# Optimization experiments

Measured on AMD Instinct MI355X. Metric: run time of the kernel, lower is better.

## Reference

```python
import jax, jax.numpy as jnp
import numpy as np

ATT_DIM = 128
C = 256
B, H, W = 4, 64, 64


def setup_inputs() -> dict:
    key = jax.random.key(0)
    ks = jax.random.split(key, 6)
    s = 1.0 / np.sqrt(C)
    return {
        "x": jax.random.normal(ks[0], (B, C, H, W), dtype=jnp.float32),
        "Wg": jax.random.normal(ks[1], (ATT_DIM, C), dtype=jnp.float32) * s,
        "Wf": jax.random.normal(ks[2], (ATT_DIM, C), dtype=jnp.float32) * s,
        "Wh": jax.random.normal(ks[3], (ATT_DIM, C), dtype=jnp.float32) * s,
        "Wv": jax.random.normal(ks[4], (C, ATT_DIM), dtype=jnp.float32) * (1.0 / np.sqrt(ATT_DIM)),
        "lambda_att": jax.random.normal(ks[5], (), dtype=jnp.float32),
    }


def reference(x, Wg, Wf, Wh, Wv, lambda_att):
    # x: [B, C, H, W]; 1x1 channels_first convs == channel matmuls
    b, c, h, w = x.shape
    hw = h * w
    d = Wg.shape[0]
    # project and flatten spatial dims -> tokens: [B, HW, d]
    g = jnp.einsum('dc,bchw->bhwd', Wg, x).reshape(b, hw, d)  # query
    f = jnp.einsum('dc,bchw->bhwd', Wf, x).reshape(b, hw, d)  # value
    hh = jnp.einsum('dc,bchw->bhwd', Wh, x).reshape(b, hw, d)  # key
    # keras layers.Attention([g, f, h]): scores = query @ key^T (unscaled),
    # out = softmax(scores) @ value
    scores = jnp.einsum('bqd,bkd->bqk', g, hh)  # [B, HW, HW]
    attw = jax.nn.softmax(scores, axis=-1)
    v = jnp.einsum('bqk,bkd->bqd', attw, f)  # [B, HW, d]
    # back to [B, d, H, W], project to C channels
    v = v.transpose(0, 2, 1).reshape(b, d, h, w)
    v = jnp.einsum('cd,bdhw->bchw', Wv, v)
    return x + lambda_att * v
```

## Files before the change

### kernel.cpp

```cpp
#include <hip/hip_runtime.h>

typedef _Float16 h16;
typedef __attribute__((ext_vector_type(8))) _Float16 half8;
typedef __attribute__((ext_vector_type(4))) _Float16 half4;
typedef __attribute__((ext_vector_type(4))) float f32x4;
typedef unsigned int u32;
typedef unsigned short u16;
typedef unsigned long long u64;

#define LOG2E 1.44269504088896340736f

__device__ __forceinline__ void gl_lds16(const void* g, void* l){
  __builtin_amdgcn_global_load_lds((const __attribute__((address_space(1))) u32*)g,
                                   (__attribute__((address_space(3))) u32*)l, 16, 0, 0);
}
__device__ __forceinline__ f32x4 mfma16(half8 a, half8 b, f32x4 c){
  return __builtin_amdgcn_mfma_f32_16x16x32_f16(a, b, c, 0, 0, 0);
}
__device__ __forceinline__ f32x4 fzero(){
  f32x4 z = {0.f, 0.f, 0.f, 0.f};
  return z;
}

__global__ void k_cvtw(const float* __restrict__ Wg, const float* __restrict__ Wf,
                       const float* __restrict__ Wh, const float* __restrict__ Wv,
                       h16* __restrict__ o){
  int i = blockIdx.x * 256 + threadIdx.x;
  o[i]          = (h16)Wg[i];
  o[32768 + i]  = (h16)Wf[i];
  o[65536 + i]  = (h16)Wh[i];
  o[98304 + i]  = (h16)Wv[i];
}

__global__ __launch_bounds__(256, 2)
void k_proj(const float* __restrict__ x, const h16* __restrict__ Wgb,
            const h16* __restrict__ Whb, const h16* __restrict__ Wfb,
            h16* __restrict__ Q, h16* __restrict__ K, h16* __restrict__ Vt){
  __shared__ __align__(16) char Xl[32 * 512];
  int bid = blockIdx.x;
  int b = bid >> 7, p0 = (bid & 127) * 32;
  int tid = threadIdx.x;
  int w = tid >> 6, lane = tid & 63, g4 = lane >> 4, ln = lane & 15;

  #pragma unroll
  for (int pass = 0; pass < 2; ++pass){
    int idx = pass * 256 + tid;
    int c4 = idx >> 3, p4 = idx & 7;
    const float* xp = x + ((size_t)b * 256 + c4 * 4) * 4096 + p0 + p4 * 4;
    float4 v0 = *(const float4*)(xp);
    float4 v1 = *(const float4*)(xp + 4096);
    float4 v2 = *(const float4*)(xp + 8192);
    float4 v3 = *(const float4*)(xp + 12288);
    #pragma unroll
    for (int i = 0; i < 4; ++i){
      int row = p4 * 4 + i;
      half4 v = { (h16)((&v0.x)[i]), (h16)((&v1.x)[i]),
                  (h16)((&v2.x)[i]), (h16)((&v3.x)[i]) };
      *(half4*)&Xl[row * 512 + ((c4 * 8) ^ ((row & 7) << 4))] = v;
    }
  }
  __syncthreads();

  half8 xf[2][8];
  #pragma unroll
  for (int pt = 0; pt < 2; ++pt){
    int p = pt * 16 + ln;
    #pragma unroll
    for (int ks = 0; ks < 8; ++ks)
      xf[pt][ks] = *(const half8*)&Xl[p * 512 + (((ks * 4 + g4) ^ (p & 7)) << 4)];
  }

  const h16* Ws0[3] = {Wgb, Whb, Wfb};
  #pragma unroll
  for (int mat = 0; mat < 3; ++mat){
    const h16* Wm = Ws0[mat];
    #pragma unroll
    for (int dtl = 0; dtl < 2; ++dtl){
      int drow = w * 32 + dtl * 16 + ln;
      half8 wf[8];
      #pragma unroll
      for (int ks = 0; ks < 8; ++ks)
        wf[ks] = *(const half8*)&Wm[(size_t)drow * 256 + ks * 32 + g4 * 8];
      #pragma unroll
      for (int pt = 0; pt < 2; ++pt){
        f32x4 acc = fzero();
        #pragma unroll
        for (int ks = 0; ks < 8; ++ks)
          acc = mfma16(wf[ks], xf[pt][ks], acc);
        int p = p0 + pt * 16 + ln;
        int dbase = w * 32 + dtl * 16 + g4 * 4;
        if (mat < 2){
          h16* Dst = (mat == 0) ? Q : K;
          half4 v = { (h16)acc[0], (h16)acc[1], (h16)acc[2], (h16)acc[3] };
          *(half4*)&Dst[((size_t)b * 4096 + p) * 128 + dbase] = v;
        } else {
          #pragma unroll
          for (int r = 0; r < 4; ++r)
            Vt[((size_t)b * 128 + dbase + r) * 4096 + p] = (h16)acc[r];
        }
      }
    }
  }
}

__global__ __launch_bounds__(256, 2)
void k_attn(const h16* __restrict__ Q, const h16* __restrict__ K,
            const h16* __restrict__ Vt, h16* __restrict__ Opart,
            float* __restrict__ Mb, float* __restrict__ Lb){
  __shared__ __align__(16) char Kl[2][16384];
  __shared__ __align__(16) char Vl[2][16384];
  __shared__ __align__(16) char Pl[4][4096];

  int bid = blockIdx.x;
  int b = bid >> 7, qb = (bid >> 2) & 31, sp = bid & 3;
  int tid = threadIdx.x;
  int w = tid >> 6, lane = tid & 63, g4 = lane >> 4, ln = lane & 15;
  int q0 = qb * 128 + w * 32;

  half8 qf[2][4];
  #pragma unroll
  for (int qt = 0; qt < 2; ++qt)
    #pragma unroll
    for (int ks = 0; ks < 4; ++ks)
      qf[qt][ks] = *(const half8*)&Q[((size_t)b * 4096 + q0 + qt * 16 + ln) * 128 + ks * 32 + g4 * 8];

  f32x4 acc[2][8];
  #pragma unroll
  for (int qt = 0; qt < 2; ++qt)
    #pragma unroll
    for (int dt = 0; dt < 8; ++dt)
      acc[qt][dt] = fzero();
  float mrow[2] = {-1e30f, -1e30f};
  float lrow[2] = {0.f, 0.f};

  int base0 = sp * 1024;

  auto stage = [&](int buf, int kv0){
    #pragma unroll
    for (int i = 0; i < 4; ++i){
      int off = i * 4096 + w * 1024 + lane * 16;
      int row = off >> 8, c16 = (off >> 4) & 15;
      gl_lds16(&K[((size_t)b * 4096 + kv0 + row) * 128 + ((c16 ^ (row & 7)) << 3)],
               &Kl[buf][i * 4096 + w * 1024]);
    }
    #pragma unroll
    for (int i = 0; i < 4; ++i){
      int off = i * 4096 + w * 1024 + lane * 16;
      int row = off >> 7, c16 = (off >> 4) & 7;
      gl_lds16(&Vt[((size_t)b * 128 + row) * 4096 + kv0 + ((c16 ^ (row & 7)) << 3)],
               &Vl[buf][i * 4096 + w * 1024]);
    }
  };

  stage(0, base0);
  __syncthreads();

  int cur = 0;
  for (int t = 0; t < 16; ++t){
    if (t < 15) stage(cur ^ 1, base0 + (t + 1) * 64);

    f32x4 s[4][2];
    #pragma unroll
    for (int kt = 0; kt < 4; ++kt)
      #pragma unroll
      for (int qt = 0; qt < 2; ++qt) s[kt][qt] = fzero();
    #pragma unroll
    for (int kt = 0; kt < 4; ++kt){
      int key = kt * 16 + ln;
      #pragma unroll
      for (int ks = 0; ks < 4; ++ks){
        half8 kf = *(const half8*)&Kl[cur][key * 256 + (((ks * 4 + g4) ^ (key & 7)) << 4)];
        #pragma unroll
        for (int qt = 0; qt < 2; ++qt)
          s[kt][qt] = mfma16(kf, qf[qt][ks], s[kt][qt]);
      }
    }

    #pragma unroll
    for (int qt = 0; qt < 2; ++qt){
      float mx = -1e30f;
      #pragma unroll
      for (int kt = 0; kt < 4; ++kt)
        #pragma unroll
        for (int r = 0; r < 4; ++r) mx = fmaxf(mx, s[kt][qt][r]);
      mx = fmaxf(mx, __shfl_xor(mx, 16));
      mx = fmaxf(mx, __shfl_xor(mx, 32));
      float mnew = fmaxf(mrow[qt], mx);
      float scale = exp2f((mrow[qt] - mnew) * LOG2E);
      mrow[qt] = mnew;
      float ps = 0.f;
      int q = qt * 16 + ln;
      #pragma unroll
      for (int kt = 0; kt < 4; ++kt){
        float e0 = exp2f((s[kt][qt][0] - mnew) * LOG2E);
        float e1 = exp2f((s[kt][qt][1] - mnew) * LOG2E);
        float e2 = exp2f((s[kt][qt][2] - mnew) * LOG2E);
        float e3 = exp2f((s[kt][qt][3] - mnew) * LOG2E);
        ps += (e0 + e1) + (e2 + e3);
        half4 pv = { (h16)e0, (h16)e1, (h16)e2, (h16)e3 };
        *(half4*)&Pl[w][q * 128 + ((kt * 32 + g4 * 8) ^ ((q & 7) << 4))] = pv;
      }
      ps += __shfl_xor(ps, 16);
      ps += __shfl_xor(ps, 32);
      lrow[qt] = lrow[qt] * scale + ps;
      #pragma unroll
      for (int r = 0; r < 4; ++r){
        float sc = __shfl(scale, g4 * 4 + r);
        #pragma unroll
        for (int dt = 0; dt < 8; ++dt) acc[qt][dt][r] *= sc;
      }
    }

    #pragma unroll
    for (int st = 0; st < 2; ++st){
      half8 pa[2];
      #pragma unroll
      for (int qt = 0; qt < 2; ++qt){
        int q = qt * 16 + ln;
        pa[qt] = *(const half8*)&Pl[w][q * 128 + (((st * 4 + g4) ^ (q & 7)) << 4)];
      }
      #pragma unroll
      for (int dt = 0; dt < 8; ++dt){
        int row = dt * 16 + ln;
        half8 vf = *(const half8*)&Vl[cur][row * 128 + (((st * 4 + g4) ^ (row & 7)) << 4)];
        #pragma unroll
        for (int qt = 0; qt < 2; ++qt)
          acc[qt][dt] = mfma16(pa[qt], vf, acc[qt][dt]);
      }
    }

    __syncthreads();
    cur ^= 1;
  }

  int pb = (b * 64 + qb * 2 + (w >> 1)) * 4 + sp;
  #pragma unroll
  for (int qt = 0; qt < 2; ++qt)
    #pragma unroll
    for (int dt = 0; dt < 8; ++dt)
      #pragma unroll
      for (int r = 0; r < 4; ++r){
        int qloc = (w & 1) * 32 + qt * 16 + g4 * 4 + r;
        Opart[(size_t)pb * 8192 + qloc * 128 + dt * 16 + ln] = (h16)acc[qt][dt][r];
      }
  if (lane < 16){
    #pragma unroll
    for (int qt = 0; qt < 2; ++qt){
      int qloc = (w & 1) * 32 + qt * 16 + lane;
      Mb[pb * 64 + qloc] = mrow[qt];
      Lb[pb * 64 + qloc] = lrow[qt];
    }
  }
}

__global__ __launch_bounds__(256, 4)
void k_comb(const h16* __restrict__ Opart, const float* __restrict__ Mb,
            const float* __restrict__ Lb, h16* __restrict__ O){
  int bid = blockIdx.x;
  int b = bid >> 6, qb = bid & 63;
  int tid = threadIdx.x;
  int q = tid >> 2, dg = tid & 3;
  int base = bid * 4;
  float m0 = Mb[(base + 0) * 64 + q], m1 = Mb[(base + 1) * 64 + q];
  float m2 = Mb[(base + 2) * 64 + q], m3 = Mb[(base + 3) * 64 + q];
  float mmax = fmaxf(fmaxf(m0, m1), fmaxf(m2, m3));
  float w0 = exp2f((m0 - mmax) * LOG2E), w1 = exp2f((m1 - mmax) * LOG2E);
  float w2 = exp2f((m2 - mmax) * LOG2E), w3 = exp2f((m3 - mmax) * LOG2E);
  float denom = w0 * Lb[(base + 0) * 64 + q] + w1 * Lb[(base + 1) * 64 + q]
              + w2 * Lb[(base + 2) * 64 + q] + w3 * Lb[(base + 3) * 64 + q];
  float inv = 1.f / denom;
  #pragma unroll
  for (int d8 = 0; d8 < 4; ++d8){
    int d = dg * 32 + d8 * 8;
    half8 a0 = *(const half8*)&Opart[((size_t)(base + 0) * 64 + q) * 128 + d];
    half8 a1 = *(const half8*)&Opart[((size_t)(base + 1) * 64 + q) * 128 + d];
    half8 a2 = *(const half8*)&Opart[((size_t)(base + 2) * 64 + q) * 128 + d];
    half8 a3 = *(const half8*)&Opart[((size_t)(base + 3) * 64 + q) * 128 + d];
    half8 o;
    #pragma unroll
    for (int j = 0; j < 8; ++j){
      float v = w0 * (float)a0[j] + w1 * (float)a1[j]
              + w2 * (float)a2[j] + w3 * (float)a3[j];
      o[j] = (h16)(v * inv);
    }
    *(half8*)&O[((size_t)b * 4096 + qb * 64 + q) * 128 + d] = o;
  }
}

__global__ __launch_bounds__(256, 2)
void k_oproj(const float* __restrict__ x, const h16* __restrict__ Wvb,
             const h16* __restrict__ O, const float* __restrict__ lamp,
             float* __restrict__ y){
  __shared__ __align__(16) char Ol[8192];
  int bid = blockIdx.x;
  int b = bid >> 7, p0 = (bid & 127) * 32;
  int tid = threadIdx.x;
  int w = tid >> 6, lane = tid & 63, g4 = lane >> 4, ln = lane & 15;
  float lam = lamp[0];

  #pragma unroll
  for (int i = 0; i < 2; ++i){
    int off = i * 4096 + w * 1024 + lane * 16;
    int row = off >> 8, c16 = (off >> 4) & 15;
    gl_lds16(&O[((size_t)b * 4096 + p0 + row) * 128 + ((c16 ^ (row & 7)) << 3)],
             &Ol[i * 4096 + w * 1024]);
  }
  __syncthreads();

  half8 of[2][4];
  #pragma unroll
  for (int pt = 0; pt < 2; ++pt){
    int p = pt * 16 + ln;
    #pragma unroll
    for (int ks = 0; ks < 4; ++ks)
      of[pt][ks] = *(const half8*)&Ol[p * 256 + (((ks * 4 + g4) ^ (p & 7)) << 4)];
  }
  #pragma unroll
  for (int ctl = 0; ctl < 4; ++ctl){
    int crow = w * 64 + ctl * 16 + ln;
    half8 wf[4];
    #pragma unroll
    for (int ks = 0; ks < 4; ++ks)
      wf[ks] = *(const half8*)&Wvb[(size_t)crow * 128 + ks * 32 + g4 * 8];
    #pragma unroll
    for (int pt = 0; pt < 2; ++pt){
      f32x4 a = fzero();
      #pragma unroll
      for (int ks = 0; ks < 4; ++ks) a = mfma16(wf[ks], of[pt][ks], a);
      int p = p0 + pt * 16 + ln;
      int c = w * 64 + ctl * 16 + g4 * 4;
      #pragma unroll
      for (int r = 0; r < 4; ++r){
        size_t idx = ((size_t)b * 256 + c + r) * 4096 + p;
        y[idx] = x[idx] + lam * a[r];
      }
    }
  }
}

extern "C" void kernel_launch(void* const* d_in, const int* in_sizes, int n_in,
                              void* d_out, int out_size, void* d_ws, size_t ws_size,
                              hipStream_t stream) {
  const float* x   = (const float*)d_in[0];
  const float* Wg  = (const float*)d_in[1];
  const float* Wf  = (const float*)d_in[2];
  const float* Wh  = (const float*)d_in[3];
  const float* Wv  = (const float*)d_in[4];
  const float* lam = (const float*)d_in[5];

  h16* Wall  = (h16*)d_ws;
  h16* Qb    = Wall + 131072;
  h16* Kb    = Qb + 2097152;
  h16* Vtb   = Kb + 2097152;
  h16* Ob    = Vtb + 2097152;
  h16* Opart = Ob + 2097152;
  float* Mb  = (float*)(Opart + 8388608);
  float* Lb  = Mb + 65536;

  k_cvtw<<<128, 256, 0, stream>>>(Wg, Wf, Wh, Wv, Wall);
  k_proj<<<512, 256, 0, stream>>>(x, Wall , Wall + 65536 , Wall + 32768 ,
                                  Qb, Kb, Vtb);
  k_attn<<<512, 256, 0, stream>>>(Qb, Kb, Vtb, Opart, Mb, Lb);
  k_comb<<<256, 256, 0, stream>>>(Opart, Mb, Lb, Ob);
  k_oproj<<<512, 256, 0, stream>>>(x, Wall + 98304 , Ob, lam, (float*)d_out);
}
```

Measured before the change: 168.0 us.

## Fuse weight conversion and split-KV combine into projection kernels, lazy softmax rescale

Removes the separate weight-conversion kernel by converting fp32 weights to fp16 inline in the projection kernels. It also removes the split-KV combine kernel by folding the partial-output merge into the output projection. Attention partials are pre-normalized, and the online-softmax rescale is skipped unless the running max grows by more than a threshold. The attention loop is unrolled by two to use static buffer indices, and projection tiles are doubled to 64 pixels per block, halving the grid. The trade-offs are two fewer launches and no intermediate O buffer, against redundant weight loads and conversions per block and lower occupancy from the halved projection grid.

After: 177.1 us. 1.05x slower.

```diff
diff --git a/kernel.cpp b/kernel.cpp
--- a/kernel.cpp
+++ b/kernel.cpp
@@ -5,7 +5,6 @@
 typedef __attribute__((ext_vector_type(4))) _Float16 half4;
 typedef __attribute__((ext_vector_type(4))) float f32x4;
 typedef unsigned int u32;
-typedef unsigned short u16;
 typedef unsigned long long u64;
 
 #define LOG2E 1.44269504088896340736f
@@ -21,31 +20,26 @@
   f32x4 z = {0.f, 0.f, 0.f, 0.f};
   return z;
 }
-
-__global__ void k_cvtw(const float* __restrict__ Wg, const float* __restrict__ Wf,
-                       const float* __restrict__ Wh, const float* __restrict__ Wv,
-                       h16* __restrict__ o){
-  int i = blockIdx.x * 256 + threadIdx.x;
-  o[i]          = (h16)Wg[i];
-  o[32768 + i]  = (h16)Wf[i];
-  o[65536 + i]  = (h16)Wh[i];
-  o[98304 + i]  = (h16)Wv[i];
+__device__ __forceinline__ half8 cvt8(const float* p){
+  half8 r = { (h16)p[0], (h16)p[1], (h16)p[2], (h16)p[3],
+              (h16)p[4], (h16)p[5], (h16)p[6], (h16)p[7] };
+  return r;
 }
 
 __global__ __launch_bounds__(256, 2)
-void k_proj(const float* __restrict__ x, const h16* __restrict__ Wgb,
-            const h16* __restrict__ Whb, const h16* __restrict__ Wfb,
+void k_proj(const float* __restrict__ x, const float* __restrict__ Wg32,
+            const float* __restrict__ Wh32, const float* __restrict__ Wf32,
             h16* __restrict__ Q, h16* __restrict__ K, h16* __restrict__ Vt){
-  __shared__ __align__(16) char Xl[32 * 512];
+  __shared__ __align__(16) char Xl[64 * 512];
   int bid = blockIdx.x;
-  int b = bid >> 7, p0 = (bid & 127) * 32;
+  int b = bid >> 6, p0 = (bid & 63) * 64;
   int tid = threadIdx.x;
   int w = tid >> 6, lane = tid & 63, g4 = lane >> 4, ln = lane & 15;
 
   #pragma unroll
-  for (int pass = 0; pass < 2; ++pass){
+  for (int pass = 0; pass < 4; ++pass){
     int idx = pass * 256 + tid;
-    int c4 = idx >> 3, p4 = idx & 7;
+    int c4 = idx >> 4, p4 = idx & 15;
     const float* xp = x + ((size_t)b * 256 + c4 * 4) * 4096 + p0 + p4 * 4;
     float4 v0 = *(const float4*)(xp);
     float4 v1 = *(const float4*)(xp + 4096);
@@ -61,28 +55,28 @@
   }
   __syncthreads();
 
-  half8 xf[2][8];
-  #pragma unroll
-  for (int pt = 0; pt < 2; ++pt){
+  half8 xf[4][8];
+  #pragma unroll
+  for (int pt = 0; pt < 4; ++pt){
     int p = pt * 16 + ln;
     #pragma unroll
     for (int ks = 0; ks < 8; ++ks)
       xf[pt][ks] = *(const half8*)&Xl[p * 512 + (((ks * 4 + g4) ^ (p & 7)) << 4)];
   }
 
-  const h16* Ws0[3] = {Wgb, Whb, Wfb};
+  const float* Ws0[3] = {Wg32, Wh32, Wf32};
   #pragma unroll
   for (int mat = 0; mat < 3; ++mat){
-    const h16* Wm = Ws0[mat];
+    const float* Wm = Ws0[mat];
     #pragma unroll
     for (int dtl = 0; dtl < 2; ++dtl){
       int drow = w * 32 + dtl * 16 + ln;
       half8 wf[8];
       #pragma unroll
       for (int ks = 0; ks < 8; ++ks)
-        wf[ks] = *(const half8*)&Wm[(size_t)drow * 256 + ks * 32 + g4 * 8];
-      #pragma unroll
-      for (int pt = 0; pt < 2; ++pt){
+        wf[ks] = cvt8(&Wm[(size_t)drow * 256 + ks * 32 + g4 * 8]);
+      #pragma unroll
+      for (int pt = 0; pt < 4; ++pt){
         f32x4 acc = fzero();
         #pragma unroll
         for (int ks = 0; ks < 8; ++ks)
@@ -135,114 +129,124 @@
 
   int base0 = sp * 1024;
 
-  auto stage = [&](int buf, int kv0){
+  auto stage = [&](char* kd, char* vd, int kv0){
     #pragma unroll
     for (int i = 0; i < 4; ++i){
       int off = i * 4096 + w * 1024 + lane * 16;
       int row = off >> 8, c16 = (off >> 4) & 15;
       gl_lds16(&K[((size_t)b * 4096 + kv0 + row) * 128 + ((c16 ^ (row & 7)) << 3)],
-               &Kl[buf][i * 4096 + w * 1024]);
+               kd + i * 4096 + w * 1024);
     }
     #pragma unroll
     for (int i = 0; i < 4; ++i){
       int off = i * 4096 + w * 1024 + lane * 16;
       int row = off >> 7, c16 = (off >> 4) & 7;
       gl_lds16(&Vt[((size_t)b * 128 + row) * 4096 + kv0 + ((c16 ^ (row & 7)) << 3)],
-               &Vl[buf][i * 4096 + w * 1024]);
+               vd + i * 4096 + w * 1024);
     }
   };
 
-  stage(0, base0);
+  stage(&Kl[0][0], &Vl[0][0], base0);
   __syncthreads();
 
-  int cur = 0;
-  for (int t = 0; t < 16; ++t){
-    if (t < 15) stage(cur ^ 1, base0 + (t + 1) * 64);
-
-    f32x4 s[4][2];
-    #pragma unroll
-    for (int kt = 0; kt < 4; ++kt)
-      #pragma unroll
-      for (int qt = 0; qt < 2; ++qt) s[kt][qt] = fzero();
-    #pragma unroll
-    for (int kt = 0; kt < 4; ++kt){
-      int key = kt * 16 + ln;
-      #pragma unroll
-      for (int ks = 0; ks < 4; ++ks){
-        half8 kf = *(const half8*)&Kl[cur][key * 256 + (((ks * 4 + g4) ^ (key & 7)) << 4)];
-        #pragma unroll
-        for (int qt = 0; qt < 2; ++qt)
-          s[kt][qt] = mfma16(kf, qf[qt][ks], s[kt][qt]);
-      }
-    }
-
-    #pragma unroll
-    for (int qt = 0; qt < 2; ++qt){
-      float mx = -1e30f;
+  for (int t2 = 0; t2 < 8; ++t2){
+    #pragma unroll
+    for (int h = 0; h < 2; ++h){
+      int t = t2 * 2 + h;
+      int kv0 = base0 + t * 64;
+      if ((h == 0) | (t2 < 7))
+        stage(&Kl[1 - h][0], &Vl[1 - h][0], kv0 + 64);
+
+      f32x4 s[4][2];
       #pragma unroll
       for (int kt = 0; kt < 4; ++kt)
         #pragma unroll
-        for (int r = 0; r < 4; ++r) mx = fmaxf(mx, s[kt][qt][r]);
-      mx = fmaxf(mx, __shfl_xor(mx, 16));
-      mx = fmaxf(mx, __shfl_xor(mx, 32));
-      float mnew = fmaxf(mrow[qt], mx);
-      float scale = exp2f((mrow[qt] - mnew) * LOG2E);
-      mrow[qt] = mnew;
-      float ps = 0.f;
-      int q = qt * 16 + ln;
+        for (int qt = 0; qt < 2; ++qt) s[kt][qt] = fzero();
       #pragma unroll
       for (int kt = 0; kt < 4; ++kt){
-        float e0 = exp2f((s[kt][qt][0] - mnew) * LOG2E);
-        float e1 = exp2f((s[kt][qt][1] - mnew) * LOG2E);
-        float e2 = exp2f((s[kt][qt][2] - mnew) * LOG2E);
-        float e3 = exp2f((s[kt][qt][3] - mnew) * LOG2E);
-        ps += (e0 + e1) + (e2 + e3);
-        half4 pv = { (h16)e0, (h16)e1, (h16)e2, (h16)e3 };
-        *(half4*)&Pl[w][q * 128 + ((kt * 32 + g4 * 8) ^ ((q & 7) << 4))] = pv;
-      }
-      ps += __shfl_xor(ps, 16);
-      ps += __shfl_xor(ps, 32);
-      lrow[qt] = lrow[qt] * scale + ps;
-      #pragma unroll
-      for (int r = 0; r < 4; ++r){
-        float sc = __shfl(scale, g4 * 4 + r);
-        #pragma unroll
-        for (int dt = 0; dt < 8; ++dt) acc[qt][dt][r] *= sc;
-      }
-    }
-
-    #pragma unroll
-    for (int st = 0; st < 2; ++st){
-      half8 pa[2];
+        int key = kt * 16 + ln;
+        #pragma unroll
+        for (int ks = 0; ks < 4; ++ks){
+          half8 kf = *(const half8*)&Kl[h][key * 256 + (((ks * 4 + g4) ^ (key & 7)) << 4)];
+          #pragma unroll
+          for (int qt = 0; qt < 2; ++qt)
+            s[kt][qt] = mfma16(kf, qf[qt][ks], s[kt][qt]);
+        }
+      }
+
       #pragma unroll
       for (int qt = 0; qt < 2; ++qt){
+        float mx = -1e30f;
+        #pragma unroll
+        for (int kt = 0; kt < 4; ++kt)
+          #pragma unroll
+          for (int r = 0; r < 4; ++r) mx = fmaxf(mx, s[kt][qt][r]);
+        mx = fmaxf(mx, __shfl_xor(mx, 16));
+        mx = fmaxf(mx, __shfl_xor(mx, 32));
+        if (!__all(mx <= mrow[qt] + 8.f)){
+          float mnew = fmaxf(mrow[qt], mx);
+          float scale = exp2f((mrow[qt] - mnew) * LOG2E);
+          lrow[qt] *= scale;
+          #pragma unroll
+          for (int r = 0; r < 4; ++r){
+            float sc = __shfl(scale, g4 * 4 + r);
+            #pragma unroll
+            for (int dt = 0; dt < 8; ++dt) acc[qt][dt][r] *= sc;
+          }
+          mrow[qt] = mnew;
+        }
+        float ps = 0.f;
         int q = qt * 16 + ln;
-        pa[qt] = *(const half8*)&Pl[w][q * 128 + (((st * 4 + g4) ^ (q & 7)) << 4)];
-      }
-      #pragma unroll
-      for (int dt = 0; dt < 8; ++dt){
-        int row = dt * 16 + ln;
-        half8 vf = *(const half8*)&Vl[cur][row * 128 + (((st * 4 + g4) ^ (row & 7)) << 4)];
-        #pragma unroll
-        for (int qt = 0; qt < 2; ++qt)
-          acc[qt][dt] = mfma16(pa[qt], vf, acc[qt][dt]);
-      }
-    }
-
-    __syncthreads();
-    cur ^= 1;
+        #pragma unroll
+        for (int kt = 0; kt < 4; ++kt){
+          float e0 = exp2f((s[kt][qt][0] - mrow[qt]) * LOG2E);
+          float e1 = exp2f((s[kt][qt][1] - mrow[qt]) * LOG2E);
+          float e2 = exp2f((s[kt][qt][2] - mrow[qt]) * LOG2E);
+          float e3 = exp2f((s[kt][qt][3] - mrow[qt]) * LOG2E);
+          ps += (e0 + e1) + (e2 + e3);
+          half4 pv = { (h16)e0, (h16)e1, (h16)e2, (h16)e3 };
+          *(half4*)&Pl[w][q * 128 + ((kt * 32 + g4 * 8) ^ ((q & 7) << 4))] = pv;
+        }
+        ps += __shfl_xor(ps, 16);
+        ps += __shfl_xor(ps, 32);
+        lrow[qt] += ps;
+      }
+
+      #pragma unroll
+      for (int st = 0; st < 2; ++st){
+        half8 pa[2];
+        #pragma unroll
+        for (int qt = 0; qt < 2; ++qt){
+          int q = qt * 16 + ln;
+          pa[qt] = *(const half8*)&Pl[w][q * 128 + (((st * 4 + g4) ^ (q & 7)) << 4)];
+        }
+        #pragma unroll
+        for (int dt = 0; dt < 8; ++dt){
+          int row = dt * 16 + ln;
+          half8 vf = *(const half8*)&Vl[h][row * 128 + (((st * 4 + g4) ^ (row & 7)) << 4)];
+          #pragma unroll
+          for (int qt = 0; qt < 2; ++qt)
+            acc[qt][dt] = mfma16(pa[qt], vf, acc[qt][dt]);
+        }
+      }
+
+      __syncthreads();
+    }
   }
 
   int pb = (b * 64 + qb * 2 + (w >> 1)) * 4 + sp;
   #pragma unroll
-  for (int qt = 0; qt < 2; ++qt)
-    #pragma unroll
-    for (int dt = 0; dt < 8; ++dt)
-      #pragma unroll
-      for (int r = 0; r < 4; ++r){
-        int qloc = (w & 1) * 32 + qt * 16 + g4 * 4 + r;
-        Opart[(size_t)pb * 8192 + qloc * 128 + dt * 16 + ln] = (h16)acc[qt][dt][r];
-      }
+  for (int qt = 0; qt < 2; ++qt){
+    float inv = 1.f / lrow[qt];
+    #pragma unroll
+    for (int r = 0; r < 4; ++r){
+      float invr = __shfl(inv, g4 * 4 + r);
+      int qloc = (w & 1) * 32 + qt * 16 + g4 * 4 + r;
+      #pragma unroll
+      for (int dt = 0; dt < 8; ++dt)
+        Opart[(size_t)pb * 8192 + qloc * 128 + dt * 16 + ln] = (h16)(acc[qt][dt][r] * invr);
+    }
+  }
   if (lane < 16){
     #pragma unroll
     for (int qt = 0; qt < 2; ++qt){
@@ -253,77 +257,57 @@
   }
 }
 
-__global__ __launch_bounds__(256, 4)
-void k_comb(const h16* __restrict__ Opart, const float* __restrict__ Mb,
-            const float* __restrict__ Lb, h16* __restrict__ O){
+__global__ __launch_bounds__(256, 2)
+void k_oproj(const float* __restrict__ x, const float* __restrict__ Wv32,
+             const h16* __restrict__ Opart, const float* __restrict__ Mb,
+             const float* __restrict__ Lb, const float* __restrict__ lamp,
+             float* __restrict__ y){
   int bid = blockIdx.x;
-  int b = bid >> 6, qb = bid & 63;
-  int tid = threadIdx.x;
-  int q = tid >> 2, dg = tid & 3;
-  int base = bid * 4;
-  float m0 = Mb[(base + 0) * 64 + q], m1 = Mb[(base + 1) * 64 + q];
-  float m2 = Mb[(base + 2) * 64 + q], m3 = Mb[(base + 3) * 64 + q];
-  float mmax = fmaxf(fmaxf(m0, m1), fmaxf(m2, m3));
-  float w0 = exp2f((m0 - mmax) * LOG2E), w1 = exp2f((m1 - mmax) * LOG2E);
-  float w2 = exp2f((m2 - mmax) * LOG2E), w3 = exp2f((m3 - mmax) * LOG2E);
-  float denom = w0 * Lb[(base + 0) * 64 + q] + w1 * Lb[(base + 1) * 64 + q]
-              + w2 * Lb[(base + 2) * 64 + q] + w3 * Lb[(base + 3) * 64 + q];
-  float inv = 1.f / denom;
-  #pragma unroll
-  for (int d8 = 0; d8 < 4; ++d8){
-    int d = dg * 32 + d8 * 8;
-    half8 a0 = *(const half8*)&Opart[((size_t)(base + 0) * 64 + q) * 128 + d];
-    half8 a1 = *(const half8*)&Opart[((size_t)(base + 1) * 64 + q) * 128 + d];
-    half8 a2 = *(const half8*)&Opart[((size_t)(base + 2) * 64 + q) * 128 + d];
-    half8 a3 = *(const half8*)&Opart[((size_t)(base + 3) * 64 + q) * 128 + d];
-    half8 o;
-    #pragma unroll
-    for (int j = 0; j < 8; ++j){
-      float v = w0 * (float)a0[j] + w1 * (float)a1[j]
-              + w2 * (float)a2[j] + w3 * (float)a3[j];
-      o[j] = (h16)(v * inv);
-    }
-    *(half8*)&O[((size_t)b * 4096 + qb * 64 + q) * 128 + d] = o;
-  }
-}
-
-__global__ __launch_bounds__(256, 2)
-void k_oproj(const float* __restrict__ x, const h16* __restrict__ Wvb,
-             const h16* __restrict__ O, const float* __restrict__ lamp,
-             float* __restrict__ y){
-  __shared__ __align__(16) char Ol[8192];
-  int bid = blockIdx.x;
-  int b = bid >> 7, p0 = (bid & 127) * 32;
+  int b = bid >> 6, g64 = bid & 63;
+  int p0 = g64 * 64;
   int tid = threadIdx.x;
   int w = tid >> 6, lane = tid & 63, g4 = lane >> 4, ln = lane & 15;
   float lam = lamp[0];
-
-  #pragma unroll
-  for (int i = 0; i < 2; ++i){
-    int off = i * 4096 + w * 1024 + lane * 16;
-    int row = off >> 8, c16 = (off >> 4) & 15;
-    gl_lds16(&O[((size_t)b * 4096 + p0 + row) * 128 + ((c16 ^ (row & 7)) << 3)],
-             &Ol[i * 4096 + w * 1024]);
-  }
-  __syncthreads();
-
-  half8 of[2][4];
-  #pragma unroll
-  for (int pt = 0; pt < 2; ++pt){
+  int base = (b * 64 + g64) * 4;
+
+  half8 of[4][4];
+  #pragma unroll
+  for (int pt = 0; pt < 4; ++pt){
     int p = pt * 16 + ln;
-    #pragma unroll
-    for (int ks = 0; ks < 4; ++ks)
-      of[pt][ks] = *(const half8*)&Ol[p * 256 + (((ks * 4 + g4) ^ (p & 7)) << 4)];
-  }
+    float m0 = Mb[(base + 0) * 64 + p], m1 = Mb[(base + 1) * 64 + p];
+    float m2 = Mb[(base + 2) * 64 + p], m3 = Mb[(base + 3) * 64 + p];
+    float mmax = fmaxf(fmaxf(m0, m1), fmaxf(m2, m3));
+    float w0 = exp2f((m0 - mmax) * LOG2E) * Lb[(base + 0) * 64 + p];
+    float w1 = exp2f((m1 - mmax) * LOG2E) * Lb[(base + 1) * 64 + p];
+    float w2 = exp2f((m2 - mmax) * LOG2E) * Lb[(base + 2) * 64 + p];
+    float w3 = exp2f((m3 - mmax) * LOG2E) * Lb[(base + 3) * 64 + p];
+    float inv = 1.f / (w0 + w1 + w2 + w3);
+    w0 *= inv; w1 *= inv; w2 *= inv; w3 *= inv;
+    #pragma unroll
+    for (int ks = 0; ks < 4; ++ks){
+      size_t eo = (size_t)p * 128 + ks * 32 + g4 * 8;
+      half8 a0 = *(const half8*)&Opart[(size_t)(base + 0) * 8192 + eo];
+      half8 a1 = *(const half8*)&Opart[(size_t)(base + 1) * 8192 + eo];
+      half8 a2 = *(const half8*)&Opart[(size_t)(base + 2) * 8192 + eo];
+      half8 a3 = *(const half8*)&Opart[(size_t)(base + 3) * 8192 + eo];
+      half8 o;
+      #pragma unroll
+      for (int j = 0; j < 8; ++j)
+        o[j] = (h16)(w0 * (float)a0[j] + w1 * (float)a1[j]
+                   + w2 * (float)a2[j] + w3 * (float)a3[j]);
+      of[pt][ks] = o;
+    }
+  }
+
   #pragma unroll
   for (int ctl = 0; ctl < 4; ++ctl){
     int crow = w * 64 + ctl * 16 + ln;
     half8 wf[4];
     #pragma unroll
     for (int ks = 0; ks < 4; ++ks)
-      wf[ks] = *(const half8*)&Wvb[(size_t)crow * 128 + ks * 32 + g4 * 8];
-    #pragma unroll
-    for (int pt = 0; pt < 2; ++pt){
+      wf[ks] = cvt8(&Wv32[(size_t)crow * 128 + ks * 32 + g4 * 8]);
+    #pragma unroll
+    for (int pt = 0; pt < 4; ++pt){
       f32x4 a = fzero();
       #pragma unroll
       for (int ks = 0; ks < 4; ++ks) a = mfma16(wf[ks], of[pt][ks], a);
@@ -348,19 +332,14 @@
   const float* Wv  = (const float*)d_in[4];
   const float* lam = (const float*)d_in[5];
 
-  h16* Wall  = (h16*)d_ws;
-  h16* Qb    = Wall + 131072;
+  h16* Qb    = (h16*)d_ws;
   h16* Kb    = Qb + 2097152;
   h16* Vtb   = Kb + 2097152;
-  h16* Ob    = Vtb + 2097152;
-  h16* Opart = Ob + 2097152;
+  h16* Opart = Vtb + 2097152;
   float* Mb  = (float*)(Opart + 8388608);
   float* Lb  = Mb + 65536;
 
-  k_cvtw<<<128, 256, 0, stream>>>(Wg, Wf, Wh, Wv, Wall);
-  k_proj<<<512, 256, 0, stream>>>(x, Wall , Wall + 65536 , Wall + 32768 ,
-                                  Qb, Kb, Vtb);
+  k_proj<<<256, 256, 0, stream>>>(x, Wg, Wh, Wf, Qb, Kb, Vtb);
   k_attn<<<512, 256, 0, stream>>>(Qb, Kb, Vtb, Opart, Mb, Lb);
-  k_comb<<<256, 256, 0, stream>>>(Opart, Mb, Lb, Ob);
-  k_oproj<<<512, 256, 0, stream>>>(x, Wall + 98304 , Ob, lam, (float*)d_out);
-}
+  k_oproj<<<256, 256, 0, stream>>>(x, Wv, Opart, Mb, Lb, lam, (float*)d_out);
+}
```
